# Kernel optimization log

Hardware: AMD Instinct MI355X
Metric: run time of the kernel (lower is better)

## Reference

```python
import jax, jax.numpy as jnp
import numpy as np

N, K, D = 262144, 1024, 64


def setup_inputs() -> dict:
    key = jax.random.key(0)
    kx, kc = jax.random.split(key)
    x = jax.random.normal(kx, (N, D), dtype=jnp.float32)
    # codebook init in torch: rand * 0.2 - 0.1  (uniform in [-0.1, 0.1])
    codebook = jax.random.uniform(kc, (K, D), dtype=jnp.float32) * 0.2 - 0.1
    return {"x": x, "codebook": codebook}


def reference(x, codebook):
    x_sq = jnp.sum(x * x, axis=-1, keepdims=True)          # [N, 1]
    c_sq = jnp.sum(codebook * codebook, axis=-1)           # [K]
    distances = x_sq - 2.0 * (x @ codebook.T) + c_sq[None, :]  # [N, K]
    Z = jnp.argmin(distances, axis=-1)                     # [N] int
    q = codebook[Z]                                        # [N, D] gather
    q_with_st = x + jax.lax.stop_gradient(q - x)
    vq_loss = jnp.mean((jax.lax.stop_gradient(q) - x) ** 2)
    commitment_loss = jnp.mean((jax.lax.stop_gradient(x) - q) ** 2)
    return (Z, q_with_st, (vq_loss, commitment_loss))
```

## Files before the change

kernel.cpp:

```cpp
#include <hip/hip_runtime.h>
#include <math.h>
#include <limits.h>


static constexpr int NROWS = 262144;
static constexpr int KC    = 1024;
static constexpr int DIM   = 64;
static constexpr int CAP   = 65536;

static constexpr size_t CSQ_OFF    = 0;
static constexpr size_t CSPRE_OFF  = 4096;
static constexpr size_t CSPLIT_OFF = 8192;
static constexpr size_t CTR_OFF    = 139264;
static constexpr size_t LIST_OFF   = 139268;
static constexpr size_t PART_OFF   = 401416;

static constexpr float BIGC = 83886080.0f;

typedef __attribute__((ext_vector_type(8)))  _Float16 half8;
typedef __attribute__((ext_vector_type(16))) float    f32x16;

static __device__ __forceinline__ unsigned umin(unsigned a, unsigned b) { return a < b ? a : b; }
static __device__ __forceinline__ unsigned umax(unsigned a, unsigned b) { return a > b ? a : b; }

__global__ __launch_bounds__(64) void prep_kernel(const float* __restrict__ cb,
                                                  float* __restrict__ csq,
                                                  float* __restrict__ cspre,
                                                  unsigned short* __restrict__ cs,
                                                  float4* __restrict__ cbt4,
                                                  int* __restrict__ counter) {
#pragma clang fp contract(off)
    if (blockIdx.x == 0 && threadIdx.x == 0) *counter = 0;
    const int c = blockIdx.x * 64 + threadIdx.x;
    const float4* row = reinterpret_cast<const float4*>(cb + (size_t)c * DIM);
    float e[64];
#pragma unroll
    for (int q = 0; q < 16; ++q) {
        float4 v = row[q];
        cbt4[q * 1024 + c] = v;
        e[q * 4 + 0] = v.x; e[q * 4 + 1] = v.y;
        e[q * 4 + 2] = v.z; e[q * 4 + 3] = v.w;
    }
    float r[8];
#pragma unroll
    for (int g = 0; g < 8; ++g)
#pragma unroll
        for (int j = 0; j < 8; ++j) {
            float sq = e[8 * g + j] * e[8 * g + j];
            if (g == 0) r[j] = sq; else r[j] += sq;
        }
    float s = ((r[0] + r[1]) + (r[2] + r[3])) + ((r[4] + r[5]) + (r[6] + r[7]));
    csq[c]   = s;
    cspre[c] = 65536.0f * s + BIGC;

    const int sub = c >> 6, c_l = c & 63;
    unsigned short* base = cs + (size_t)sub * 4096 + (size_t)c_l * 8;
#pragma unroll
    for (int g = 0; g < 8; ++g) {
        half8 hv;
#pragma unroll
        for (int j = 0; j < 8; ++j)
            hv[j] = (_Float16)(e[8 * g + j] * -131072.0f);
        *reinterpret_cast<half8*>(base + g * 512) = hv;
    }
}

#define STAGE(buf_, chk_) do {                                                          \
    const char* _s = (const char*)csplit + (size_t)(chk_) * 8192                        \
                     + (size_t)(w * 2) * 1024 + (size_t)lane * 16;                      \
    char* _d = (char*)(&bbuf[buf_][0]) + (size_t)(w * 2) * 1024;                        \
    _Pragma("unroll")                                                                   \
    for (int _it = 0; _it < 2; ++_it)                                                   \
        __builtin_amdgcn_global_load_lds(                                               \
            (const __attribute__((address_space(1))) unsigned int*)(_s + _it * 1024),   \
            (__attribute__((address_space(3))) unsigned int*)(_d + _it * 1024),         \
            16, 0, 0);                                                                  \
} while (0)

__global__ __launch_bounds__(256, 4) void vq_mfma_kernel(
        const float* __restrict__ x, const unsigned short* __restrict__ csplit,
        const float* __restrict__ cspre_g, float* __restrict__ zout,
        int* __restrict__ counter, int* __restrict__ list) {
    __shared__ unsigned short bbuf[2][4096];
    __shared__ float cspre_s[1024];

    const int tid  = threadIdx.x;
    const int w    = tid >> 6;
    const int lane = tid & 63;
    const int h    = lane >> 5;
    const int cl5  = lane & 31;
    const int rowbase = blockIdx.x * 128 + w * 32;

    STAGE(0, 0);
    {
        float4 v = reinterpret_cast<const float4*>(cspre_g)[tid];
        reinterpret_cast<float4*>(cspre_s)[tid] = v;
    }

    half8 xh[4], xl[4];
    float sa;
    {
        const float* xrow = x + (size_t)(rowbase + cl5) * DIM;
        float s = 0.0f;
#pragma unroll
        for (int j = 0; j < 4; ++j) {
            float4 p0 = *reinterpret_cast<const float4*>(xrow + j * 16 + h * 8);
            float4 p1 = *reinterpret_cast<const float4*>(xrow + j * 16 + h * 8 + 4);
            float v[8] = {p0.x, p0.y, p0.z, p0.w, p1.x, p1.y, p1.z, p1.w};
#pragma unroll
            for (int e = 0; e < 8; ++e) {
                float f = v[e];
                s += fabsf(f);
                _Float16 hx = (_Float16)f;
                float fh = (float)hx;
                xh[j][e] = hx;
                xl[j][e] = (_Float16)(f - fh);
            }
        }
        sa = s + __shfl_xor(s, 32, 64);
    }
    __syncthreads();

    unsigned k1 = 0xFFFFFFFFu, k2 = 0xFFFFFFFFu;
    const int lofs = cl5 * 16 + h * 1024;
    static constexpr int IDX[16] = {0,1,2,3, 8,9,10,11, 16,17,18,19, 24,25,26,27};

    for (int chk = 0; chk < 16; ++chk) {
        const int cur = chk & 1;
        if (chk < 15) STAGE(cur ^ 1, chk + 1);
        const char* bb = (const char*)(&bbuf[cur][0]);
#pragma unroll
        for (int t = 0; t < 2; ++t) {
            const unsigned cbase = (unsigned)(chk * 64 + t * 32 + 4 * h);
            const float* cp = &cspre_s[chk * 64 + t * 32 + 4 * h];
            float4 g0 = *reinterpret_cast<const float4*>(cp);
            float4 g1 = *reinterpret_cast<const float4*>(cp + 8);
            float4 g2 = *reinterpret_cast<const float4*>(cp + 16);
            float4 g3 = *reinterpret_cast<const float4*>(cp + 24);
            f32x16 ini;
            ini[0]  = g0.x; ini[1]  = g0.y; ini[2]  = g0.z; ini[3]  = g0.w;
            ini[4]  = g1.x; ini[5]  = g1.y; ini[6]  = g1.z; ini[7]  = g1.w;
            ini[8]  = g2.x; ini[9]  = g2.y; ini[10] = g2.z; ini[11] = g2.w;
            ini[12] = g3.x; ini[13] = g3.y; ini[14] = g3.z; ini[15] = g3.w;

            const char* bp = bb + t * 512 + lofs;
            f32x16 a0;
            {
                half8 bch = *reinterpret_cast<const half8*>(bp);
                a0 = __builtin_amdgcn_mfma_f32_32x32x16_f16(bch, xh[0], ini, 0, 0, 0);
                a0 = __builtin_amdgcn_mfma_f32_32x32x16_f16(bch, xl[0], a0, 0, 0, 0);
            }
#pragma unroll
            for (int j = 1; j < 4; ++j) {
                half8 bch = *reinterpret_cast<const half8*>(bp + j * 2048);
                a0 = __builtin_amdgcn_mfma_f32_32x32x16_f16(bch, xh[j], a0, 0, 0, 0);
                a0 = __builtin_amdgcn_mfma_f32_32x32x16_f16(bch, xl[j], a0, 0, 0, 0);
            }
#pragma unroll
            for (int p = 0; p < 8; ++p) {
                const int r = 2 * p, r2 = 2 * p + 1;
                unsigned ka = (__float_as_uint(a0[r])  << 10) + cbase + IDX[r];
                unsigned kb = (__float_as_uint(a0[r2]) << 10) + cbase + IDX[r2];
                unsigned pmin = umin(ka, kb), pmax = umax(ka, kb);
                unsigned tt = umax(pmin, k1);
                k2 = umin(umin(k2, tt), pmax);
                k1 = umin(k1, pmin);
            }
        }
        __syncthreads();
    }

    {
        unsigned o1 = (unsigned)__shfl_xor((int)k1, 32, 64);
        unsigned o2 = (unsigned)__shfl_xor((int)k2, 32, 64);
        unsigned mn = umin(k1, o1), mx = umax(k1, o1);
        unsigned K1 = mn;
        unsigned K2 = umin(umin(k2, o2), mx);
        if (h == 0) {
            const int row = rowbase + cl5;
            zout[row] = (float)(K1 & 1023u);
            unsigned Tq = (unsigned)(8192.0f * (1.2e-4f * sa + 1.4e-3f)) + 2u;
            if ((K2 - K1) < (Tq << 10)) {
                int id = atomicAdd(counter, 1);
                if (id < CAP) list[id] = row;
            }
        }
    }
}

__global__ __launch_bounds__(256) void rescore_kernel(
        const float* __restrict__ x, const float4* __restrict__ cbt4,
        const float* __restrict__ csq, const int* __restrict__ counter,
        const int* __restrict__ list, float* __restrict__ zout) {
#pragma clang fp contract(off)
    __shared__ float xs[8][64];
    __shared__ float xsq_s[8];
    __shared__ float bv[4][8];
    __shared__ int   bix[4][8];
    const int tid  = threadIdx.x;
    const int lane = tid & 63;
    const int w    = tid >> 6;
    int cnt = *counter; if (cnt > CAP) cnt = CAP;

    for (int base = blockIdx.x * 8; base < cnt; base += gridDim.x * 8) {
        if (tid < 128) {
            int r  = tid >> 4, q = tid & 15;
            int li = base + r; if (li >= cnt) li = cnt - 1;
            int row = list[li];
            float4 v = reinterpret_cast<const float4*>(x + (size_t)row * DIM)[q];
            *reinterpret_cast<float4*>(&xs[r][q * 4]) = v;
        }
        __syncthreads();
        if (tid < 8) {
            float r8[8];
#pragma unroll
            for (int g = 0; g < 8; ++g)
#pragma unroll
                for (int j = 0; j < 8; ++j) {
                    float xv = xs[tid][8 * g + j];
                    float sq = xv * xv;
                    if (g == 0) r8[j] = sq; else r8[j] += sq;
                }
            xsq_s[tid] = ((r8[0] + r8[1]) + (r8[2] + r8[3]))
                       + ((r8[4] + r8[5]) + (r8[6] + r8[7]));
        }
        __syncthreads();

        float bmv[8]; int bmi[8];
#pragma unroll
        for (int r = 0; r < 8; ++r) { bmv[r] = INFINITY; bmi[r] = 0; }

#pragma clang loop unroll(disable)
        for (int cc = 0; cc < 4; ++cc) {
            const int c = cc * 256 + tid;
            float dot[8];
#pragma unroll
            for (int r = 0; r < 8; ++r) dot[r] = 0.0f;
#pragma clang loop unroll(disable)
            for (int q = 0; q < 16; ++q) {
                const float4 cv = cbt4[q * 1024 + c];
#pragma unroll
                for (int r = 0; r < 8; ++r) {
                    float4 xv = *reinterpret_cast<const float4*>(&xs[r][q * 4]);
                    dot[r] = __builtin_fmaf(cv.x, xv.x, dot[r]);
                    dot[r] = __builtin_fmaf(cv.y, xv.y, dot[r]);
                    dot[r] = __builtin_fmaf(cv.z, xv.z, dot[r]);
                    dot[r] = __builtin_fmaf(cv.w, xv.w, dot[r]);
                }
            }
            const float cs = csq[c];
#pragma unroll
            for (int r = 0; r < 8; ++r) {
                float dist = (xsq_s[r] - 2.0f * dot[r]) + cs;
                if (dist < bmv[r]) { bmv[r] = dist; bmi[r] = c; }
            }
        }

#pragma unroll
        for (int r = 0; r < 8; ++r) {
#pragma unroll
            for (int m = 1; m <= 32; m <<= 1) {
                float ov = __shfl_xor(bmv[r], m, 64);
                int   oi = __shfl_xor(bmi[r], m, 64);
                if (ov < bmv[r] || (ov == bmv[r] && oi < bmi[r])) {
                    bmv[r] = ov; bmi[r] = oi;
                }
            }
            if (lane == 0) { bv[w][r] = bmv[r]; bix[w][r] = bmi[r]; }
        }
        __syncthreads();
        if (tid < 8) {
            float v = bv[0][tid]; int ix = bix[0][tid];
#pragma unroll
            for (int k = 1; k < 4; ++k)
                if (bv[k][tid] < v || (bv[k][tid] == v && bix[k][tid] < ix)) {
                    v = bv[k][tid]; ix = bix[k][tid];
                }
            int li = base + tid;
            if (li < cnt) zout[list[li]] = (float)ix;
        }
        __syncthreads();
    }
}

__global__ __launch_bounds__(256) void epilogue_kernel(
        const float* __restrict__ x, const float* __restrict__ cb,
        const float* __restrict__ zf, float* __restrict__ qout,
        double* __restrict__ partial) {
#pragma clang fp contract(off)
    const int gid = blockIdx.x * 256 + threadIdx.x;
    const int row = gid >> 2;
    const int d0  = (gid & 3) * 16;
    const float4* xr = reinterpret_cast<const float4*>(x + (size_t)row * DIM + d0);
    const int z = (int)zf[row];
    const float4* qr = reinterpret_cast<const float4*>(cb + (size_t)z * DIM + d0);
    float4* op = reinterpret_cast<float4*>(qout + (size_t)row * DIM + d0);

    float lf = 0.0f;
#pragma unroll
    for (int q = 0; q < 4; ++q) {
        float4 xv = xr[q];
        float4 qv = qr[q];
        float da = qv.x - xv.x, db = qv.y - xv.y, dc = qv.z - xv.z, dd = qv.w - xv.w;
        float4 o;
        o.x = xv.x + da; o.y = xv.y + db; o.z = xv.z + dc; o.w = xv.w + dd;
        op[q] = o;
        lf += da * da; lf += db * db; lf += dc * dc; lf += dd * dd;
    }
    double lsum = (double)lf;
#pragma unroll
    for (int s = 32; s >= 1; s >>= 1) lsum += __shfl_down(lsum, s, 64);
    __shared__ double wsum[4];
    const int lane = threadIdx.x & 63, wid = threadIdx.x >> 6;
    if (lane == 0) wsum[wid] = lsum;
    __syncthreads();
    if (threadIdx.x == 0)
        partial[blockIdx.x] = (wsum[0] + wsum[1]) + (wsum[2] + wsum[3]);
}

__global__ void finalize_kernel(const double* __restrict__ partial,
                                float* __restrict__ losses) {
    double s = 0.0;
    int lane = threadIdx.x;
    for (int i = lane; i < 4096; i += 64) s += partial[i];
#pragma unroll
    for (int sh = 32; sh >= 1; sh >>= 1) s += __shfl_down(s, sh, 64);
    if (lane == 0) {
        float v = (float)(s / 16777216.0);
        losses[0] = v;
        losses[1] = v;
    }
}

extern "C" void kernel_launch(void* const* d_in, const int* in_sizes, int n_in,
                              void* d_out, int out_size, void* d_ws, size_t ws_size,
                              hipStream_t stream) {
    const float* x  = (const float*)d_in[0];
    const float* cb = (const float*)d_in[1];
    float* out    = (float*)d_out;
    float* zout   = out;
    float* qout   = out + NROWS;
    float* losses = out + NROWS + (size_t)NROWS * DIM;

    float*          csq     = (float*)((char*)d_ws + CSQ_OFF);
    float*          cspre   = (float*)((char*)d_ws + CSPRE_OFF);
    unsigned short* csplit  = (unsigned short*)((char*)d_ws + CSPLIT_OFF);
    int*            counter = (int*)((char*)d_ws + CTR_OFF);
    int*            list    = (int*)((char*)d_ws + LIST_OFF);
    double*         partial = (double*)((char*)d_ws + PART_OFF);

    float4* cbt4 = (float4*)qout;

    prep_kernel<<<16, 64, 0, stream>>>(cb, csq, cspre, csplit, cbt4, counter);
    vq_mfma_kernel<<<NROWS / 128, 256, 0, stream>>>(x, csplit, cspre, zout, counter, list);
    rescore_kernel<<<1024, 256, 0, stream>>>(x, cbt4, csq, counter, list, zout);
    epilogue_kernel<<<(NROWS * 4) / 256, 256, 0, stream>>>(x, cb, zout, qout, partial);
    finalize_kernel<<<1, 64, 0, stream>>>(partial, losses);
}
```

Before: 171.9 us.

## Load codebook fragments directly from global memory instead of LDS double-buffering

```diff
diff --git a/kernel.cpp b/kernel.cpp
--- a/kernel.cpp
+++ b/kernel.cpp
@@ -65,23 +65,10 @@
     }
 }
 
-#define STAGE(buf_, chk_) do {                                                          \
-    const char* _s = (const char*)csplit + (size_t)(chk_) * 8192                        \
-                     + (size_t)(w * 2) * 1024 + (size_t)lane * 16;                      \
-    char* _d = (char*)(&bbuf[buf_][0]) + (size_t)(w * 2) * 1024;                        \
-    _Pragma("unroll")                                                                   \
-    for (int _it = 0; _it < 2; ++_it)                                                   \
-        __builtin_amdgcn_global_load_lds(                                               \
-            (const __attribute__((address_space(1))) unsigned int*)(_s + _it * 1024),   \
-            (__attribute__((address_space(3))) unsigned int*)(_d + _it * 1024),         \
-            16, 0, 0);                                                                  \
-} while (0)
-
 __global__ __launch_bounds__(256, 4) void vq_mfma_kernel(
         const float* __restrict__ x, const unsigned short* __restrict__ csplit,
         const float* __restrict__ cspre_g, float* __restrict__ zout,
         int* __restrict__ counter, int* __restrict__ list) {
-    __shared__ unsigned short bbuf[2][4096];
     __shared__ float cspre_s[1024];
 
     const int tid  = threadIdx.x;
@@ -91,7 +78,6 @@
     const int cl5  = lane & 31;
     const int rowbase = blockIdx.x * 128 + w * 32;
 
-    STAGE(0, 0);
     {
         float4 v = reinterpret_cast<const float4*>(cspre_g)[tid];
         reinterpret_cast<float4*>(cspre_s)[tid] = v;
@@ -125,49 +111,47 @@
     const int lofs = cl5 * 16 + h * 1024;
     static constexpr int IDX[16] = {0,1,2,3, 8,9,10,11, 16,17,18,19, 24,25,26,27};
 
-    for (int chk = 0; chk < 16; ++chk) {
-        const int cur = chk & 1;
-        if (chk < 15) STAGE(cur ^ 1, chk + 1);
-        const char* bb = (const char*)(&bbuf[cur][0]);
-#pragma unroll
-        for (int t = 0; t < 2; ++t) {
-            const unsigned cbase = (unsigned)(chk * 64 + t * 32 + 4 * h);
-            const float* cp = &cspre_s[chk * 64 + t * 32 + 4 * h];
-            float4 g0 = *reinterpret_cast<const float4*>(cp);
-            float4 g1 = *reinterpret_cast<const float4*>(cp + 8);
-            float4 g2 = *reinterpret_cast<const float4*>(cp + 16);
-            float4 g3 = *reinterpret_cast<const float4*>(cp + 24);
-            f32x16 ini;
-            ini[0]  = g0.x; ini[1]  = g0.y; ini[2]  = g0.z; ini[3]  = g0.w;
-            ini[4]  = g1.x; ini[5]  = g1.y; ini[6]  = g1.z; ini[7]  = g1.w;
-            ini[8]  = g2.x; ini[9]  = g2.y; ini[10] = g2.z; ini[11] = g2.w;
-            ini[12] = g3.x; ini[13] = g3.y; ini[14] = g3.z; ini[15] = g3.w;
-
-            const char* bp = bb + t * 512 + lofs;
-            f32x16 a0;
-            {
-                half8 bch = *reinterpret_cast<const half8*>(bp);
-                a0 = __builtin_amdgcn_mfma_f32_32x32x16_f16(bch, xh[0], ini, 0, 0, 0);
-                a0 = __builtin_amdgcn_mfma_f32_32x32x16_f16(bch, xl[0], a0, 0, 0, 0);
-            }
-#pragma unroll
-            for (int j = 1; j < 4; ++j) {
-                half8 bch = *reinterpret_cast<const half8*>(bp + j * 2048);
-                a0 = __builtin_amdgcn_mfma_f32_32x32x16_f16(bch, xh[j], a0, 0, 0, 0);
-                a0 = __builtin_amdgcn_mfma_f32_32x32x16_f16(bch, xl[j], a0, 0, 0, 0);
-            }
-#pragma unroll
-            for (int p = 0; p < 8; ++p) {
-                const int r = 2 * p, r2 = 2 * p + 1;
-                unsigned ka = (__float_as_uint(a0[r])  << 10) + cbase + IDX[r];
-                unsigned kb = (__float_as_uint(a0[r2]) << 10) + cbase + IDX[r2];
-                unsigned pmin = umin(ka, kb), pmax = umax(ka, kb);
-                unsigned tt = umax(pmin, k1);
-                k2 = umin(umin(k2, tt), pmax);
-                k1 = umin(k1, pmin);
-            }
-        }
-        __syncthreads();
+#pragma clang loop unroll_count(2)
+    for (int tile = 0; tile < 32; ++tile) {
+        const unsigned cbase = (unsigned)(tile * 32 + 4 * h);
+        const float* cp = &cspre_s[tile * 32 + 4 * h];
+        float4 g0 = *reinterpret_cast<const float4*>(cp);
+        float4 g1 = *reinterpret_cast<const float4*>(cp + 8);
+        float4 g2 = *reinterpret_cast<const float4*>(cp + 16);
+        float4 g3 = *reinterpret_cast<const float4*>(cp + 24);
+        f32x16 ini;
+        ini[0]  = g0.x; ini[1]  = g0.y; ini[2]  = g0.z; ini[3]  = g0.w;
+        ini[4]  = g1.x; ini[5]  = g1.y; ini[6]  = g1.z; ini[7]  = g1.w;
+        ini[8]  = g2.x; ini[9]  = g2.y; ini[10] = g2.z; ini[11] = g2.w;
+        ini[12] = g3.x; ini[13] = g3.y; ini[14] = g3.z; ini[15] = g3.w;
+
+        const char* bp = (const char*)csplit + (size_t)(tile >> 1) * 8192
+                         + (size_t)(tile & 1) * 512 + lofs;
+        half8 b0 = *reinterpret_cast<const half8*>(bp);
+        half8 b1 = *reinterpret_cast<const half8*>(bp + 2048);
+        half8 b2 = *reinterpret_cast<const half8*>(bp + 2 * 2048);
+        half8 b3 = *reinterpret_cast<const half8*>(bp + 3 * 2048);
+
+        f32x16 a0;
+        a0 = __builtin_amdgcn_mfma_f32_32x32x16_f16(b0, xh[0], ini, 0, 0, 0);
+        a0 = __builtin_amdgcn_mfma_f32_32x32x16_f16(b0, xl[0], a0, 0, 0, 0);
+        a0 = __builtin_amdgcn_mfma_f32_32x32x16_f16(b1, xh[1], a0, 0, 0, 0);
+        a0 = __builtin_amdgcn_mfma_f32_32x32x16_f16(b1, xl[1], a0, 0, 0, 0);
+        a0 = __builtin_amdgcn_mfma_f32_32x32x16_f16(b2, xh[2], a0, 0, 0, 0);
+        a0 = __builtin_amdgcn_mfma_f32_32x32x16_f16(b2, xl[2], a0, 0, 0, 0);
+        a0 = __builtin_amdgcn_mfma_f32_32x32x16_f16(b3, xh[3], a0, 0, 0, 0);
+        a0 = __builtin_amdgcn_mfma_f32_32x32x16_f16(b3, xl[3], a0, 0, 0, 0);
+
+#pragma unroll
+        for (int p = 0; p < 8; ++p) {
+            const int r = 2 * p, r2 = 2 * p + 1;
+            unsigned ka = (__float_as_uint(a0[r])  << 10) + cbase + IDX[r];
+            unsigned kb = (__float_as_uint(a0[r2]) << 10) + cbase + IDX[r2];
+            unsigned pmin = umin(ka, kb), pmax = umax(ka, kb);
+            unsigned tt = umax(pmin, k1);
+            k2 = umin(umin(k2, tt), pmax);
+            k1 = umin(k1, pmin);
+        }
     }
 
     {
```

Result: no change. 175.0 us (+1.8%).
